# Kernel optimization log

Measured on AMD Instinct MI355X. Metric: run time of the kernel, lower is better.

## Reference

```python
import jax, jax.numpy as jnp
import numpy as np

NUM_USERS = 100000
NUM_ITEMS = 100000
D = 64
C = 9          # cat_num (9 attention layers)
B = 2048       # batch of users
L = 200        # max history length (padded with -1)
H = 16         # attention MLP hidden size


def setup_inputs() -> dict:
    key = jax.random.key(0)
    ks = jax.random.split(key, 12)
    w_range = np.sqrt(3.0 / D).astype(np.float32)

    user_inputs = jax.random.randint(ks[0], (B,), 0, NUM_USERS)
    record = jax.random.randint(ks[1], (B, L), 0, NUM_ITEMS)
    # ragged lengths: pad tail with -1 (original code breaks at -1)
    lengths = jax.random.randint(ks[2], (B, 1), L // 4, L + 1)
    record_inputs = jnp.where(jnp.arange(L)[None, :] < lengths, record, -1)
    item_inputs = jax.random.randint(ks[3], (B,), 0, NUM_ITEMS)
    item_cat = jax.random.randint(ks[4], (NUM_ITEMS,), 0, C)

    user_emb = 0.01 * jax.random.normal(ks[5], (NUM_USERS, D), jnp.float32)
    item_emb = 0.01 * jax.random.normal(ks[6], (NUM_ITEMS, D), jnp.float32)
    W1 = jax.random.uniform(ks[7], (C, H, 2 * D), jnp.float32, -w_range, w_range)
    b1 = jnp.zeros((C, H), jnp.float32)
    W2 = jax.random.uniform(ks[8], (C, 1, H), jnp.float32, -w_range, w_range)
    b2 = jnp.zeros((C, 1), jnp.float32)
    Wt1 = jax.random.uniform(ks[9], (H, 2 * D), jnp.float32, -w_range, w_range)
    bt1 = jnp.zeros((H,), jnp.float32)
    Wt2 = jax.random.uniform(ks[10], (1, H), jnp.float32, -w_range, w_range)
    bt2 = jnp.zeros((1,), jnp.float32)

    return {"user_inputs": user_inputs, "record_inputs": record_inputs,
            "item_inputs": item_inputs, "item_cat": item_cat,
            "user_emb": user_emb, "item_emb": item_emb,
            "W1": W1, "b1": b1, "W2": W2, "b2": b2,
            "Wt1": Wt1, "bt1": bt1, "Wt2": Wt2, "bt2": bt2}


def _forward(user_inputs, record_inputs, item_inputs, item_cat,
             user_emb, item_emb, W1, b1, W2, b2, Wt1, bt1, Wt2, bt2):
    tiny = jnp.asarray(1e-30, jnp.float32)
    valid = record_inputs >= 0                     # [B,L]
    rec = jnp.where(valid, record_inputs, 0)
    e = item_emb[rec]                              # [B,L,D]
    u = user_emb[user_inputs]                      # [B,D]
    x = jnp.concatenate([jnp.broadcast_to(u[:, None, :], e.shape), e], -1)  # [B,L,2D]

    # per-category attention MLP scores (C small -> compute all, gather by cat)
    h = jax.nn.relu(jnp.einsum('chi,bli->bclh', W1, x) + b1[None, :, None, :])  # [B,C,L,H]
    s = jnp.einsum('ch,bclh->bcl', W2[:, 0, :], h) + b2[:, 0][None, :, None]    # [B,C,L]

    cat = item_cat[rec]                                            # [B,L]
    member = (cat[:, None, :] == jnp.arange(C)[None, :, None]) & valid[:, None, :]  # [B,C,L]

    # masked softmax within each (user, category) group
    smax = jnp.max(jnp.where(member, s, -jnp.inf), axis=-1, keepdims=True)
    smax = jnp.where(jnp.isfinite(smax), smax, 0.0)
    z = jnp.where(member, jnp.exp(s - smax), 0.0)
    w = z / jnp.maximum(jnp.sum(z, -1, keepdims=True), tiny)       # [B,C,L]
    gvec = jnp.einsum('bcl,bld->bcd', w, e)                        # [B,C,D]
    group_has = jnp.any(member, axis=-1)                           # [B,C]

    # top-level attention over non-empty groups
    x2 = jnp.concatenate([jnp.broadcast_to(u[:, None, :], gvec.shape), gvec], -1)  # [B,C,2D]
    h2 = jax.nn.relu(jnp.einsum('hi,bci->bch', Wt1, x2) + bt1)      # [B,C,H]
    s2 = jnp.einsum('h,bch->bc', Wt2[0], h2) + bt2[0]               # [B,C]
    s2max = jnp.max(jnp.where(group_has, s2, -jnp.inf), -1, keepdims=True)
    s2max = jnp.where(jnp.isfinite(s2max), s2max, 0.0)
    z2 = jnp.where(group_has, jnp.exp(s2 - s2max), 0.0)
    w2 = z2 / jnp.maximum(jnp.sum(z2, -1, keepdims=True), tiny)
    hybrid = jnp.einsum('bc,bcd->bd', w2, gvec)                     # [B,D]

    ti = item_emb[item_inputs]                                      # [B,D]
    return jnp.sum(hybrid * ti, -1).reshape(-1, 1, 1)               # [B,1,1]


def reference(user_inputs, record_inputs, item_inputs, item_cat,
              user_emb, item_emb, W1, b1, W2, b2, Wt1, bt1, Wt2, bt2):
    return _forward(user_inputs, record_inputs, item_inputs, item_cat,
                    user_emb, item_emb, W1, b1, W2, b2, Wt1, bt1, Wt2, bt2)
```

## Files before the change

### kernel.cpp

```cpp
#include <hip/hip_runtime.h>
#include <math.h>

#define NB 2048
#define LL 200
#define PADL 256
#define DD 64
#define CC 9
#define HH 16
#define NW 4


__global__ __launch_bounds__(256) void din_ka(
    const int* __restrict__ user_inputs,
    const int* __restrict__ record_inputs,
    const int* __restrict__ item_cat,
    const float* __restrict__ user_emb,
    const float* __restrict__ W1,
    const float* __restrict__ b1,
    int* __restrict__ srow_g,
    int* __restrict__ cstart_g,
    float* __restrict__ pre_g)
{
  const int b = blockIdx.x;
  const int t = threadIdx.x;
  const int wave = t >> 6, lane = t & 63;

  __shared__ float u_s[DD];
  __shared__ int   wcnt[NW][CC];
  __shared__ int   cstart[CC + 1];
  __shared__ int   ccnt[CC];

  int r = -1, c0 = -1;
  if (t < LL) {
    r = record_inputs[b * LL + t];
    if (r >= 0) c0 = item_cat[r];
  }
  if (t < DD) u_s[t] = user_emb[(size_t)user_inputs[b] * DD + t];

  srow_g[b * PADL + t] = 0;

  int myrank = 0;
  #pragma unroll
  for (int c = 0; c < CC; ++c) {
    unsigned long long m = __ballot(c0 == c);
    if (lane == 0) wcnt[wave][c] = __popcll(m);
    if (c0 == c) myrank = __popcll(m & ((1ULL << lane) - 1ULL));
  }
  __syncthreads();

  if (t == 0) {
    int acc = 0;
    #pragma unroll
    for (int c = 0; c < CC; ++c) {
      cstart[c] = acc;
      int cn = wcnt[0][c] + wcnt[1][c] + wcnt[2][c] + wcnt[3][c];
      ccnt[c] = cn;
      acc = (acc + cn + 3) & ~3;
    }
    cstart[CC] = acc;
  }
  if (t < CC * HH) {
    int c = t / HH, j = t % HH;
    const float* wp = &W1[(size_t)(c * HH + j) * (2 * DD)];
    float acc = b1[c * HH + j];
    #pragma unroll 8
    for (int d = 0; d < DD; ++d) acc += wp[d] * u_s[d];
    pre_g[(size_t)(b * CC + c) * HH + j] = acc;
  }
  __syncthreads();

  if (c0 >= 0) {
    int off = cstart[c0];
    for (int w = 0; w < wave; ++w) off += wcnt[w][c0];
    srow_g[b * PADL + off + myrank] = r;
  }
  if (t < CC + 1) cstart_g[b * 20 + t] = cstart[t];
  else if (t < 2 * CC + 1) cstart_g[b * 20 + 10 + (t - CC - 1)] = ccnt[t - CC - 1];
}

__global__ __launch_bounds__(256) void din_kb(
    const float* __restrict__ item_emb,
    const float* __restrict__ W1,
    const float* __restrict__ W2,
    const float* __restrict__ b2,
    const int* __restrict__ srow_g,
    const int* __restrict__ cstart_g,
    const float* __restrict__ pre_g,
    float* __restrict__ z_g)
{
  const int t = threadIdx.x;

  __shared__ float4 w_lds[HH * 16 * CC];
  __shared__ float  w2_s[CC * HH];
  __shared__ float  b2_s[CC];

  #pragma unroll
  for (int k = t; k < HH * 16 * CC; k += 256) {
    int c = k >> 8;
    int ji = k & 255;
    int j = ji >> 4, i = ji & 15;
    w_lds[ji * CC + c] = ((const float4*)W1)[(size_t)(c * HH + j) * 32 + 16 + i];
  }
  if (t < CC * HH) w2_s[t] = W2[t];
  if (t < CC) b2_s[t] = b2[t];
  __syncthreads();

  const int g = blockIdx.x * 256 + t;
  const int b = g >> 6;
  const int q4 = (g & 63) * 4;
  const int* cs = &cstart_g[b * 20];
  if (q4 >= cs[CC]) return;

  int c = 0;
  #pragma unroll
  for (int q = 0; q < CC - 1; ++q) c += (q4 >= cs[q + 1]) ? 1 : 0;

  const int base = b * PADL + q4;
  const int r0 = srow_g[base + 0], r1 = srow_g[base + 1];
  const int r2 = srow_g[base + 2], r3 = srow_g[base + 3];
  const float4* e0 = (const float4*)&item_emb[(size_t)r0 * DD];
  const float4* e1 = (const float4*)&item_emb[(size_t)r1 * DD];
  const float4* e2 = (const float4*)&item_emb[(size_t)r2 * DD];
  const float4* e3 = (const float4*)&item_emb[(size_t)r3 * DD];

  float acc0[HH], acc1[HH], acc2[HH], acc3[HH];
  {
    const float4* pp = (const float4*)&pre_g[(size_t)(b * CC + c) * HH];
    #pragma unroll
    for (int jq = 0; jq < 4; ++jq) {
      float4 pv = pp[jq];
      acc0[jq*4+0] = pv.x; acc0[jq*4+1] = pv.y; acc0[jq*4+2] = pv.z; acc0[jq*4+3] = pv.w;
      acc1[jq*4+0] = pv.x; acc1[jq*4+1] = pv.y; acc1[jq*4+2] = pv.z; acc1[jq*4+3] = pv.w;
      acc2[jq*4+0] = pv.x; acc2[jq*4+1] = pv.y; acc2[jq*4+2] = pv.z; acc2[jq*4+3] = pv.w;
      acc3[jq*4+0] = pv.x; acc3[jq*4+1] = pv.y; acc3[jq*4+2] = pv.z; acc3[jq*4+3] = pv.w;
    }
  }

  #pragma unroll
  for (int i = 0; i < 16; ++i) {
    float4 a0 = e0[i], a1 = e1[i], a2 = e2[i], a3 = e3[i];
    #pragma unroll
    for (int j = 0; j < HH; ++j) {
      float4 wv = w_lds[(j * 16 + i) * CC + c];
      acc0[j] += wv.x * a0.x + wv.y * a0.y + wv.z * a0.z + wv.w * a0.w;
      acc1[j] += wv.x * a1.x + wv.y * a1.y + wv.z * a1.z + wv.w * a1.w;
      acc2[j] += wv.x * a2.x + wv.y * a2.y + wv.z * a2.z + wv.w * a2.w;
      acc3[j] += wv.x * a3.x + wv.y * a3.y + wv.z * a3.z + wv.w * a3.w;
    }
  }

  float s0 = b2_s[c], s1 = s0, s2 = s0, s3 = s0;
  #pragma unroll
  for (int j = 0; j < HH; ++j) {
    float w2v = w2_s[c * HH + j];
    s0 += w2v * fmaxf(acc0[j], 0.f);
    s1 += w2v * fmaxf(acc1[j], 0.f);
    s2 += w2v * fmaxf(acc2[j], 0.f);
    s3 += w2v * fmaxf(acc3[j], 0.f);
  }
  *(float4*)&z_g[base] = make_float4(expf(s0), expf(s1), expf(s2), expf(s3));
}

__global__ __launch_bounds__(256) void din_kc(
    const float* __restrict__ item_emb,
    const int* __restrict__ srow_g,
    const float* __restrict__ z_g,
    const int* __restrict__ cstart_g,
    float* __restrict__ gvec_g)
{
  const int pair = blockIdx.x * NW + (threadIdx.x >> 6);
  const int lane = threadIdx.x & 63;
  const int b = pair / CC;
  const int c = pair - b * CC;
  const int g = lane >> 4;
  const int h = lane & 15;

  const int i0 = cstart_g[b * 20 + c];
  const int n  = cstart_g[b * 20 + 10 + c];
  const int sb = b * PADL + i0;

  float4 acc = make_float4(0.f, 0.f, 0.f, 0.f);
  float  zs  = 0.f;

  for (int cb = 0; cb < n; cb += 64) {
    const int nn = min(64, n - cb);
    const bool ok = (cb + lane) < n;
    int   rv = ok ? srow_g[sb + cb + lane] : 0;
    float zv = ok ? z_g[sb + cb + lane]    : 0.f;
    zs += zv;

    const int kmax = (nn + 3) >> 2;
    #pragma unroll 4
    for (int k = 0; k < kmax; ++k) {
      const int j = 4 * k + g;
      const int   rr = __shfl(rv, j, 64);
      const float zz = __shfl(zv, j, 64);
      const float4 ev = *(const float4*)&item_emb[(size_t)rr * DD + 4 * h];
      acc.x += zz * ev.x; acc.y += zz * ev.y;
      acc.z += zz * ev.z; acc.w += zz * ev.w;
    }
  }

  acc.x += __shfl_xor(acc.x, 16, 64); acc.y += __shfl_xor(acc.y, 16, 64);
  acc.z += __shfl_xor(acc.z, 16, 64); acc.w += __shfl_xor(acc.w, 16, 64);
  acc.x += __shfl_xor(acc.x, 32, 64); acc.y += __shfl_xor(acc.y, 32, 64);
  acc.z += __shfl_xor(acc.z, 32, 64); acc.w += __shfl_xor(acc.w, 32, 64);
  #pragma unroll
  for (int off = 32; off > 0; off >>= 1) zs += __shfl_xor(zs, off, 64);

  if (g == 0) {
    const float inv = 1.f / fmaxf(zs, 1e-30f);
    *(float4*)&gvec_g[(size_t)pair * DD + 4 * h] =
        make_float4(acc.x * inv, acc.y * inv, acc.z * inv, acc.w * inv);
  }
}

__global__ __launch_bounds__(256) void din_kd(
    const int* __restrict__ user_inputs,
    const int* __restrict__ item_inputs,
    const float* __restrict__ user_emb,
    const float* __restrict__ item_emb,
    const float* __restrict__ Wt1,
    const float* __restrict__ bt1,
    const float* __restrict__ Wt2,
    const float* __restrict__ bt2,
    const int* __restrict__ cstart_g,
    const float* __restrict__ gvec_g,
    float* __restrict__ out)
{
  const int b = blockIdx.x;
  const int t = threadIdx.x;

  __shared__ float u_s[DD];
  __shared__ float g_s[CC * DD];
  __shared__ float h2_s[CC][HH];
  __shared__ float w2_s[CC];
  __shared__ int   cnt_s[CC];

  if (t < DD) u_s[t] = user_emb[(size_t)user_inputs[b] * DD + t];
  for (int x = t; x < CC * DD; x += 256) g_s[x] = gvec_g[(size_t)b * CC * DD + x];
  if (t < CC) cnt_s[t] = cstart_g[b * 20 + 10 + t];
  __syncthreads();

  if (t < CC * HH) {
    int c = t / HH, j = t % HH;
    const float* wp = &Wt1[(size_t)j * (2 * DD)];
    float acc = bt1[j];
    #pragma unroll 8
    for (int d = 0; d < DD; ++d) acc += wp[d] * u_s[d];
    #pragma unroll 8
    for (int d = 0; d < DD; ++d) acc += wp[DD + d] * g_s[c * DD + d];
    h2_s[c][j] = fmaxf(acc, 0.f);
  }
  __syncthreads();

  if (t == 0) {
    float s2[CC];
    float m = -INFINITY;
    #pragma unroll
    for (int c = 0; c < CC; ++c) {
      float acc = bt2[0];
      #pragma unroll
      for (int j = 0; j < HH; ++j) acc += Wt2[j] * h2_s[c][j];
      s2[c] = acc;
      if (cnt_s[c] > 0) m = fmaxf(m, acc);
    }
    if (m == -INFINITY) m = 0.f;
    float sum = 0.f;
    float z2[CC];
    #pragma unroll
    for (int c = 0; c < CC; ++c) {
      z2[c] = (cnt_s[c] > 0) ? expf(s2[c] - m) : 0.f;
      sum += z2[c];
    }
    float inv = 1.f / fmaxf(sum, 1e-30f);
    #pragma unroll
    for (int c = 0; c < CC; ++c) w2_s[c] = z2[c] * inv;
  }
  __syncthreads();

  if (t < DD) {
    float hy = 0.f;
    #pragma unroll
    for (int c = 0; c < CC; ++c) hy += w2_s[c] * g_s[c * DD + t];
    float ti = item_emb[(size_t)item_inputs[b] * DD + t];
    float prod = hy * ti;
    #pragma unroll
    for (int off = 32; off > 0; off >>= 1)
      prod += __shfl_down(prod, off, 64);
    if (t == 0) out[b] = prod;
  }
}

extern "C" void kernel_launch(void* const* d_in, const int* in_sizes, int n_in,
                              void* d_out, int out_size, void* d_ws, size_t ws_size,
                              hipStream_t stream) {
  const int*   user_inputs   = (const int*)d_in[0];
  const int*   record_inputs = (const int*)d_in[1];
  const int*   item_inputs   = (const int*)d_in[2];
  const int*   item_cat      = (const int*)d_in[3];
  const float* user_emb      = (const float*)d_in[4];
  const float* item_emb      = (const float*)d_in[5];
  const float* W1            = (const float*)d_in[6];
  const float* b1            = (const float*)d_in[7];
  const float* W2            = (const float*)d_in[8];
  const float* b2            = (const float*)d_in[9];
  const float* Wt1           = (const float*)d_in[10];
  const float* bt1           = (const float*)d_in[11];
  const float* Wt2           = (const float*)d_in[12];
  const float* bt2           = (const float*)d_in[13];
  float* out = (float*)d_out;

  char* ws = (char*)d_ws;
  int*   srow_g   = (int*)(ws);
  float* z_g      = (float*)(ws + 2097152);
  int*   cstart_g = (int*)(ws + 4194304);
  float* pre_g    = (float*)(ws + 4358144);
  float* gvec_g   = (float*)(ws + 4358144);

  din_ka<<<NB, 256, 0, stream>>>(user_inputs, record_inputs, item_cat,
                                 user_emb, W1, b1, srow_g, cstart_g, pre_g);
  din_kb<<<(NB * 64) / 256, 256, 0, stream>>>(item_emb, W1, W2, b2,
                                              srow_g, cstart_g, pre_g, z_g);
  din_kc<<<(NB * CC) / NW, 256, 0, stream>>>(item_emb, srow_g, z_g, cstart_g, gvec_g);
  din_kd<<<NB, 256, 0, stream>>>(user_inputs, item_inputs, user_emb, item_emb,
                                 Wt1, bt1, Wt2, bt2, cstart_g, gvec_g, out);
}
```

Before: 80.81 us.

## Fuse per-category scoring and weighted pooling into one wave-per-group kernel

Merges the attention-score kernel and the grouped weighted-sum kernel into a single kernel. Each wave handles one (batch, category) pair, keeps its W1 slice in registers, computes the 16 hidden pre-activations for four items at once using a butterfly shuffle transpose-reduce, and accumulates the exp-weighted embeddings directly. This removes one launch, the z_g round trip and the second gather of the item embeddings. In exchange it adds many cross-lane shuffles per item, holds 64 floats of weights per thread, and reads srow_g past n for padded lanes (masked only at the exp).

```diff
diff --git a/kernel.cpp b/kernel.cpp
--- a/kernel.cpp
+++ b/kernel.cpp
@@ -78,7 +78,7 @@
   else if (t < 2 * CC + 1) cstart_g[b * 20 + 10 + (t - CC - 1)] = ccnt[t - CC - 1];
 }
 
-__global__ __launch_bounds__(256) void din_kb(
+__global__ __launch_bounds__(256) void din_kbc(
     const float* __restrict__ item_emb,
     const float* __restrict__ W1,
     const float* __restrict__ W2,
@@ -86,127 +86,86 @@
     const int* __restrict__ srow_g,
     const int* __restrict__ cstart_g,
     const float* __restrict__ pre_g,
-    float* __restrict__ z_g)
-{
-  const int t = threadIdx.x;
-
-  __shared__ float4 w_lds[HH * 16 * CC];
-  __shared__ float  w2_s[CC * HH];
-  __shared__ float  b2_s[CC];
-
-  #pragma unroll
-  for (int k = t; k < HH * 16 * CC; k += 256) {
-    int c = k >> 8;
-    int ji = k & 255;
-    int j = ji >> 4, i = ji & 15;
-    w_lds[ji * CC + c] = ((const float4*)W1)[(size_t)(c * HH + j) * 32 + 16 + i];
-  }
-  if (t < CC * HH) w2_s[t] = W2[t];
-  if (t < CC) b2_s[t] = b2[t];
-  __syncthreads();
-
-  const int g = blockIdx.x * 256 + t;
-  const int b = g >> 6;
-  const int q4 = (g & 63) * 4;
-  const int* cs = &cstart_g[b * 20];
-  if (q4 >= cs[CC]) return;
-
-  int c = 0;
-  #pragma unroll
-  for (int q = 0; q < CC - 1; ++q) c += (q4 >= cs[q + 1]) ? 1 : 0;
-
-  const int base = b * PADL + q4;
-  const int r0 = srow_g[base + 0], r1 = srow_g[base + 1];
-  const int r2 = srow_g[base + 2], r3 = srow_g[base + 3];
-  const float4* e0 = (const float4*)&item_emb[(size_t)r0 * DD];
-  const float4* e1 = (const float4*)&item_emb[(size_t)r1 * DD];
-  const float4* e2 = (const float4*)&item_emb[(size_t)r2 * DD];
-  const float4* e3 = (const float4*)&item_emb[(size_t)r3 * DD];
-
-  float acc0[HH], acc1[HH], acc2[HH], acc3[HH];
-  {
-    const float4* pp = (const float4*)&pre_g[(size_t)(b * CC + c) * HH];
-    #pragma unroll
-    for (int jq = 0; jq < 4; ++jq) {
-      float4 pv = pp[jq];
-      acc0[jq*4+0] = pv.x; acc0[jq*4+1] = pv.y; acc0[jq*4+2] = pv.z; acc0[jq*4+3] = pv.w;
-      acc1[jq*4+0] = pv.x; acc1[jq*4+1] = pv.y; acc1[jq*4+2] = pv.z; acc1[jq*4+3] = pv.w;
-      acc2[jq*4+0] = pv.x; acc2[jq*4+1] = pv.y; acc2[jq*4+2] = pv.z; acc2[jq*4+3] = pv.w;
-      acc3[jq*4+0] = pv.x; acc3[jq*4+1] = pv.y; acc3[jq*4+2] = pv.z; acc3[jq*4+3] = pv.w;
-    }
-  }
-
-  #pragma unroll
-  for (int i = 0; i < 16; ++i) {
-    float4 a0 = e0[i], a1 = e1[i], a2 = e2[i], a3 = e3[i];
-    #pragma unroll
-    for (int j = 0; j < HH; ++j) {
-      float4 wv = w_lds[(j * 16 + i) * CC + c];
-      acc0[j] += wv.x * a0.x + wv.y * a0.y + wv.z * a0.z + wv.w * a0.w;
-      acc1[j] += wv.x * a1.x + wv.y * a1.y + wv.z * a1.z + wv.w * a1.w;
-      acc2[j] += wv.x * a2.x + wv.y * a2.y + wv.z * a2.z + wv.w * a2.w;
-      acc3[j] += wv.x * a3.x + wv.y * a3.y + wv.z * a3.z + wv.w * a3.w;
-    }
-  }
-
-  float s0 = b2_s[c], s1 = s0, s2 = s0, s3 = s0;
-  #pragma unroll
-  for (int j = 0; j < HH; ++j) {
-    float w2v = w2_s[c * HH + j];
-    s0 += w2v * fmaxf(acc0[j], 0.f);
-    s1 += w2v * fmaxf(acc1[j], 0.f);
-    s2 += w2v * fmaxf(acc2[j], 0.f);
-    s3 += w2v * fmaxf(acc3[j], 0.f);
-  }
-  *(float4*)&z_g[base] = make_float4(expf(s0), expf(s1), expf(s2), expf(s3));
-}
-
-__global__ __launch_bounds__(256) void din_kc(
-    const float* __restrict__ item_emb,
-    const int* __restrict__ srow_g,
-    const float* __restrict__ z_g,
-    const int* __restrict__ cstart_g,
     float* __restrict__ gvec_g)
 {
   const int pair = blockIdx.x * NW + (threadIdx.x >> 6);
   const int lane = threadIdx.x & 63;
+  const int g = lane >> 4;
+  const int h = lane & 15;
   const int b = pair / CC;
   const int c = pair - b * CC;
-  const int g = lane >> 4;
-  const int h = lane & 15;
 
   const int i0 = cstart_g[b * 20 + c];
   const int n  = cstart_g[b * 20 + 10 + c];
   const int sb = b * PADL + i0;
 
+  float4 Wj[HH];
+  #pragma unroll
+  for (int j = 0; j < HH; ++j)
+    Wj[j] = *(const float4*)&W1[(size_t)(c * HH + j) * (2 * DD) + DD + 4 * h];
+
+  const float pre_h = pre_g[(size_t)(b * CC + c) * HH + h];
+  const float w2h   = W2[c * HH + h];
+  const float b2c   = b2[c];
+
   float4 acc = make_float4(0.f, 0.f, 0.f, 0.f);
   float  zs  = 0.f;
 
-  for (int cb = 0; cb < n; cb += 64) {
-    const int nn = min(64, n - cb);
-    const bool ok = (cb + lane) < n;
-    int   rv = ok ? srow_g[sb + cb + lane] : 0;
-    float zv = ok ? z_g[sb + cb + lane]    : 0.f;
-    zs += zv;
-
-    const int kmax = (nn + 3) >> 2;
-    #pragma unroll 4
-    for (int k = 0; k < kmax; ++k) {
-      const int j = 4 * k + g;
-      const int   rr = __shfl(rv, j, 64);
-      const float zz = __shfl(zv, j, 64);
-      const float4 ev = *(const float4*)&item_emb[(size_t)rr * DD + 4 * h];
-      acc.x += zz * ev.x; acc.y += zz * ev.y;
-      acc.z += zz * ev.z; acc.w += zz * ev.w;
-    }
+  for (int k = 0; k < n; k += 4) {
+    const int i = k + g;
+    const int rr = srow_g[sb + i];
+    const float4 e = *(const float4*)&item_emb[(size_t)rr * DD + 4 * h];
+
+    float p[HH];
+    #pragma unroll
+    for (int j = 0; j < HH; ++j)
+      p[j] = Wj[j].x * e.x + Wj[j].y * e.y + Wj[j].z * e.z + Wj[j].w * e.w;
+
+    float q8[8];
+    #pragma unroll
+    for (int j = 0; j < 8; ++j) {
+      float keep = (h & 8) ? p[j + 8] : p[j];
+      float send = (h & 8) ? p[j]     : p[j + 8];
+      q8[j] = keep + __shfl_xor(send, 8, 64);
+    }
+    float q4v[4];
+    #pragma unroll
+    for (int j = 0; j < 4; ++j) {
+      float keep = (h & 4) ? q8[j + 4] : q8[j];
+      float send = (h & 4) ? q8[j]     : q8[j + 4];
+      q4v[j] = keep + __shfl_xor(send, 4, 64);
+    }
+    float q2v[2];
+    #pragma unroll
+    for (int j = 0; j < 2; ++j) {
+      float keep = (h & 2) ? q4v[j + 2] : q4v[j];
+      float send = (h & 2) ? q4v[j]     : q4v[j + 2];
+      q2v[j] = keep + __shfl_xor(send, 2, 64);
+    }
+    float q1;
+    {
+      float keep = (h & 1) ? q2v[1] : q2v[0];
+      float send = (h & 1) ? q2v[0] : q2v[1];
+      q1 = keep + __shfl_xor(send, 1, 64);
+    }
+
+    float v = w2h * fmaxf(q1 + pre_h, 0.f);
+    v += __shfl_xor(v, 1, 64);
+    v += __shfl_xor(v, 2, 64);
+    v += __shfl_xor(v, 4, 64);
+    v += __shfl_xor(v, 8, 64);
+
+    const float z = (i < n) ? expf(v + b2c) : 0.f;
+    acc.x += z * e.x; acc.y += z * e.y; acc.z += z * e.z; acc.w += z * e.w;
+    zs += z;
   }
 
   acc.x += __shfl_xor(acc.x, 16, 64); acc.y += __shfl_xor(acc.y, 16, 64);
   acc.z += __shfl_xor(acc.z, 16, 64); acc.w += __shfl_xor(acc.w, 16, 64);
   acc.x += __shfl_xor(acc.x, 32, 64); acc.y += __shfl_xor(acc.y, 32, 64);
   acc.z += __shfl_xor(acc.z, 32, 64); acc.w += __shfl_xor(acc.w, 32, 64);
-  #pragma unroll
-  for (int off = 32; off > 0; off >>= 1) zs += __shfl_xor(zs, off, 64);
+  zs += __shfl_xor(zs, 16, 64);
+  zs += __shfl_xor(zs, 32, 64);
 
   if (g == 0) {
     const float inv = 1.f / fmaxf(zs, 1e-30f);
@@ -313,16 +272,14 @@
 
   char* ws = (char*)d_ws;
   int*   srow_g   = (int*)(ws);
-  float* z_g      = (float*)(ws + 2097152);
+  float* pre_g    = (float*)(ws + 2097152);
   int*   cstart_g = (int*)(ws + 4194304);
-  float* pre_g    = (float*)(ws + 4358144);
   float* gvec_g   = (float*)(ws + 4358144);
 
   din_ka<<<NB, 256, 0, stream>>>(user_inputs, record_inputs, item_cat,
                                  user_emb, W1, b1, srow_g, cstart_g, pre_g);
-  din_kb<<<(NB * 64) / 256, 256, 0, stream>>>(item_emb, W1, W2, b2,
-                                              srow_g, cstart_g, pre_g, z_g);
-  din_kc<<<(NB * CC) / NW, 256, 0, stream>>>(item_emb, srow_g, z_g, cstart_g, gvec_g);
+  din_kbc<<<(NB * CC) / NW, 256, 0, stream>>>(item_emb, W1, W2, b2,
+                                              srow_g, cstart_g, pre_g, gvec_g);
   din_kd<<<NB, 256, 0, stream>>>(user_inputs, item_inputs, user_emb, item_emb,
                                  Wt1, bt1, Wt2, bt2, cstart_g, gvec_g, out);
 }
```

Measured after the change: 79.55 us. No clear change (-1.6%).
